# Optimization experiments

Hardware: AMD Instinct MI355X
Metric: run time of the kernel (lower is better)

Reference implementation:

```python
import jax, jax.numpy as jnp
import numpy as np
import math

NUM_HEADS = 8
LN_EPS = 1e-5
SINK_EPS = 1.0  # entropic eps in SinkhornDistance (eps=1)


def _layer_norm(x, g, b):
    m = jnp.mean(x, axis=-1, keepdims=True)
    v = jnp.var(x, axis=-1, keepdims=True)
    return (x - m) * jax.lax.rsqrt(v + LN_EPS) * g + b


def setup_inputs() -> dict:
    key = jax.random.key(0)
    ks = jax.random.split(key, 8)
    B, n, dQ, dV = 8, 1024, 512, 512
    s = 1.0 / math.sqrt(dV)
    return {
        "Q": jax.random.normal(ks[0], (B, n, dQ), jnp.float32),
        "K": jax.random.normal(ks[1], (B, n, dQ), jnp.float32),
        "Wq": jax.random.normal(ks[2], (dV, dQ), jnp.float32) * s,
        "bq": jax.random.normal(ks[3], (dV,), jnp.float32) * 0.01,
        "Wo": jax.random.normal(ks[4], (dV, dV), jnp.float32) * s,
        "bo": jax.random.normal(ks[5], (dV,), jnp.float32) * 0.01,
        "g0": jnp.ones((dV,), jnp.float32),
        "b0": jnp.zeros((dV,), jnp.float32),
        "g1": jnp.ones((dV,), jnp.float32),
        "b1": jnp.zeros((dV,), jnp.float32),
    }


def reference(Q, K, Wq, bq, Wo, bo, g0, b0, g1, b1):
    # K is accepted by the original forward but unused (K_ = V_ = Q_).
    B, n, _ = Q.shape
    dim_V = Wq.shape[0]
    H = NUM_HEADS
    d = dim_V // H

    Qp = Q @ Wq.T + bq                                   # [B, n, dim_V]
    # torch.cat(Q.split(d, 2), 0): head-major stacking -> [H*B, n, d]
    Q_ = Qp.reshape(B, n, H, d).transpose(2, 0, 1, 3).reshape(H * B, n, d)

    sqrtV = math.sqrt(math.sqrt(dim_V))
    X = Q_ / sqrtV
    # cost = dotmat(X, X) = -X X^T  (overall scaled by 1/sqrt(dim_V))
    C = -jnp.einsum('bnd,bmd->bnm', X, X)                # [HB, n, n]

    # log-domain Sinkhorn, eps=1, max_iter=1, mu = nu = 1/n
    log_mu = jnp.log(1.0 / n + 1e-8).astype(Q.dtype)
    M0 = -C / SINK_EPS
    u = SINK_EPS * (log_mu - jax.scipy.special.logsumexp(M0, axis=-1))         # [HB, n]
    v = SINK_EPS * (log_mu - jax.scipy.special.logsumexp(
        (-C + u[:, :, None]) / SINK_EPS, axis=1))                               # [HB, n]
    pi = jnp.exp((-C + u[:, :, None] + v[:, None, :]) / SINK_EPS)               # [HB, n, n]

    A = pi * n
    O_ = Q_ + jnp.einsum('bnm,bmd->bnd', A, Q_)          # [HB, n, d]
    # inverse head stacking -> [B, n, dim_V]
    O = O_.reshape(H, B, n, d).transpose(1, 2, 0, 3).reshape(B, n, dim_V)

    O = _layer_norm(O, g0, b0)
    O = O + jax.nn.relu(O @ Wo.T + bo)
    O = _layer_norm(O, g1, b1)
    return O
```

## Files before the change

### kernel.cpp

```cpp
#include <hip/hip_runtime.h>
#include <hip/hip_bf16.h>

typedef __bf16 bf16;
typedef __bf16 bf16x4 __attribute__((ext_vector_type(4)));
typedef __bf16 bf16x8 __attribute__((ext_vector_type(8)));
typedef float  f32x4  __attribute__((ext_vector_type(4)));

#define DEVI static __device__ __forceinline__

constexpr float SCALE_S = 0.04419417382415922f;
constexpr float LOG_MU  = -6.93146156565f;
constexpr int   LDT     = 72;

DEVI f32x4 mfma16(bf16x8 a, bf16x8 b, f32x4 c) {
    return __builtin_amdgcn_mfma_f32_16x16x32_bf16(a, b, c, 0, 0, 0);
}

DEVI bf16x8 cvt8(const float* __restrict__ p) {
    const float4 f0 = *(const float4*)p;
    const float4 f1 = *(const float4*)(p + 4);
    bf16x8 h;
    h[0] = (bf16)f0.x; h[1] = (bf16)f0.y; h[2] = (bf16)f0.z; h[3] = (bf16)f0.w;
    h[4] = (bf16)f1.x; h[5] = (bf16)f1.y; h[6] = (bf16)f1.z; h[7] = (bf16)f1.w;
    return h;
}

template<int EPI>
__global__ __launch_bounds__(256)
void gemm_kernel(const void* __restrict__ Ap, const float* __restrict__ Bm,
                 const float* __restrict__ bias, const bf16* __restrict__ X0,
                 bf16* __restrict__ outQh, bf16* __restrict__ outQhT,
                 float* __restrict__ outT)
{
    __shared__ bf16 sA[64 * LDT];
    __shared__ bf16 sB[64 * LDT];
    const int tid = threadIdx.x;
    const int rowBase = blockIdx.y * 64;
    const int colBase = blockIdx.x * 64;
    const int w = tid >> 6, lane = tid & 63, quad = lane >> 4, l16 = lane & 15;
    const int wr = (w >> 1) * 32, wc = (w & 1) * 32;

    f32x4 acc[2][2];
    #pragma unroll
    for (int i = 0; i < 2; ++i)
        #pragma unroll
        for (int j = 0; j < 2; ++j)
            #pragma unroll
            for (int e = 0; e < 4; ++e) acc[i][j][e] = 0.f;

    for (int kt = 0; kt < 512; kt += 64) {
        if (kt) __syncthreads();
        #pragma unroll
        for (int it = 0; it < 2; ++it) {
            int idx = it * 256 + tid;
            int r = idx >> 3, kb = idx & 7;
            if (EPI == 0) {
                *(bf16x8*)(&sA[r * LDT + kb * 8]) =
                    cvt8((const float*)Ap + (size_t)(rowBase + r) * 512 + kt + kb * 8);
            } else {
                *(uint4*)(&sA[r * LDT + kb * 8]) =
                    *(const uint4*)((const bf16*)Ap + (size_t)(rowBase + r) * 512 + kt + kb * 8);
            }
            *(bf16x8*)(&sB[r * LDT + kb * 8]) =
                cvt8(Bm + (size_t)(colBase + r) * 512 + kt + kb * 8);
        }
        __syncthreads();
        #pragma unroll
        for (int kk = 0; kk < 2; ++kk) {
            bf16x8 a[2], b[2];
            #pragma unroll
            for (int i = 0; i < 2; ++i)
                a[i] = *(const bf16x8*)(&sA[(wr + i * 16 + l16) * LDT + kk * 32 + quad * 8]);
            #pragma unroll
            for (int j = 0; j < 2; ++j)
                b[j] = *(const bf16x8*)(&sB[(wc + j * 16 + l16) * LDT + kk * 32 + quad * 8]);
            #pragma unroll
            for (int i = 0; i < 2; ++i)
                #pragma unroll
                for (int j = 0; j < 2; ++j)
                    acc[i][j] = mfma16(a[i], b[j], acc[i][j]);
        }
    }

    #pragma unroll
    for (int i = 0; i < 2; ++i) {
        #pragma unroll
        for (int j = 0; j < 2; ++j) {
            const int col = colBase + wc + j * 16 + l16;
            const float bv = bias[col];
            if (EPI == 0) {
                const int hh = col >> 6, jj = col & 63;
                const int rowA = rowBase + wr + i * 16 + quad * 4;
                const int bb = rowA >> 10, iib = rowA & 1023;
                const int bhh = (hh << 3) + bb;
                bf16x4 pk;
                #pragma unroll
                for (int rg = 0; rg < 4; ++rg) {
                    const float z = acc[i][j][rg] + bv;
                    pk[rg] = (bf16)z;
                    outQh[((size_t)(bhh * 1024 + iib + rg) << 6) + jj] = (bf16)z;
                }
                if (outQhT)
                    *(bf16x4*)(&outQhT[(((size_t)bhh * 64 + jj) << 10) + iib]) = pk;
            } else {
                #pragma unroll
                for (int rg = 0; rg < 4; ++rg) {
                    const int row = rowBase + wr + i * 16 + quad * 4 + rg;
                    const float z = acc[i][j][rg] + bv;
                    const float x0 = (float)X0[(size_t)row * 512 + col];
                    outT[(size_t)row * 512 + col] = x0 + fmaxf(z, 0.f);
                }
            }
        }
    }
}

template<int ADD_U>
__global__ __launch_bounds__(256, 4)
void sink_lse_kernel(const bf16* __restrict__ Qh, const float* __restrict__ uin,
                     float* __restrict__ out)
{
    __shared__ bf16 sQi[128 * LDT];
    __shared__ bf16 sQm[2][64 * LDT];
    __shared__ float su[1024];
    const int tid = threadIdx.x;
    const int bh = blockIdx.y;
    const int rowTile = blockIdx.x * 128;
    const bf16* Qb = Qh + ((size_t)bh << 16);

    #pragma unroll
    for (int it = 0; it < 4; ++it) {
        int idx = it * 256 + tid;
        int r = idx >> 3, kb = idx & 7;
        *(uint4*)(&sQi[r * LDT + kb * 8]) =
            *(const uint4*)(Qb + ((rowTile + r) << 6) + kb * 8);
    }
    if (ADD_U)
        *(float4*)(&su[tid * 4]) = *(const float4*)(uin + (bh << 10) + tid * 4);

    const int r0 = tid >> 3, kb0 = tid & 7;
    #pragma unroll
    for (int it = 0; it < 2; ++it)
        *(uint4*)(&sQm[0][(it * 32 + r0) * LDT + kb0 * 8]) =
            *(const uint4*)(Qb + ((it * 32 + r0) << 6) + kb0 * 8);
    __syncthreads();

    const int w = tid >> 6, lane = tid & 63, quad = lane >> 4, l16 = lane & 15;
    float rsum[2][4] = {{0.f,0.f,0.f,0.f},{0.f,0.f,0.f,0.f}};

    for (int mt = 0; mt < 16; ++mt) {
        const int cur = mt & 1;
        uint4 pf[2];
        if (mt < 15) {
            #pragma unroll
            for (int it = 0; it < 2; ++it)
                pf[it] = *(const uint4*)(Qb + (((mt + 1) * 64 + it * 32 + r0) << 6) + kb0 * 8);
        }

        f32x4 acc[2][4];
        #pragma unroll
        for (int a = 0; a < 2; ++a)
            #pragma unroll
            for (int ct = 0; ct < 4; ++ct)
                #pragma unroll
                for (int e = 0; e < 4; ++e) acc[a][ct][e] = 0.f;

        #pragma unroll
        for (int kk = 0; kk < 2; ++kk) {
            bf16x8 afr[2], bfr[4];
            #pragma unroll
            for (int a = 0; a < 2; ++a)
                afr[a] = *(const bf16x8*)(&sQi[(w * 32 + a * 16 + l16) * LDT + kk * 32 + quad * 8]);
            #pragma unroll
            for (int ct = 0; ct < 4; ++ct)
                bfr[ct] = *(const bf16x8*)(&sQm[cur][(ct * 16 + l16) * LDT + kk * 32 + quad * 8]);
            #pragma unroll
            for (int a = 0; a < 2; ++a)
                #pragma unroll
                for (int ct = 0; ct < 4; ++ct)
                    acc[a][ct] = mfma16(afr[a], bfr[ct], acc[a][ct]);
        }
        #pragma unroll
        for (int a = 0; a < 2; ++a)
            #pragma unroll
            for (int ct = 0; ct < 4; ++ct) {
                const float uadd = ADD_U ? su[mt * 64 + ct * 16 + l16] : 0.f;
                #pragma unroll
                for (int rg = 0; rg < 4; ++rg)
                    rsum[a][rg] += __expf(acc[a][ct][rg] * SCALE_S + uadd);
            }

        if (mt < 15) {
            #pragma unroll
            for (int it = 0; it < 2; ++it)
                *(uint4*)(&sQm[cur ^ 1][(it * 32 + r0) * LDT + kb0 * 8]) = pf[it];
        }
        __syncthreads();
    }
    #pragma unroll
    for (int off = 1; off < 16; off <<= 1)
        #pragma unroll
        for (int a = 0; a < 2; ++a)
            #pragma unroll
            for (int rg = 0; rg < 4; ++rg)
                rsum[a][rg] += __shfl_xor(rsum[a][rg], off);

    if (l16 == 0) {
        #pragma unroll
        for (int a = 0; a < 2; ++a)
            #pragma unroll
            for (int rg = 0; rg < 4; ++rg)
                out[(bh << 10) + rowTile + w * 32 + a * 16 + quad * 4 + rg] =
                    LOG_MU - __logf(rsum[a][rg]);
    }
}

template<int USE_T>
__global__ __launch_bounds__(256, 2)
void sink_av_kernel(const bf16* __restrict__ Qh, const bf16* __restrict__ QhT,
                    const float* __restrict__ u, const float* __restrict__ v,
                    float* __restrict__ O)
{
    __shared__ bf16 sQi[128 * LDT];
    __shared__ bf16 sQm[2][64 * LDT];
    __shared__ bf16 sQmT[2][64 * LDT];
    __shared__ bf16 sP[4][32 * LDT];
    __shared__ float sv[1024];
    const int tid = threadIdx.x;
    const int bh = blockIdx.y;
    const int rowTile = blockIdx.x * 128;
    const bf16* Qb = Qh + ((size_t)bh << 16);
    const bf16* QbT = QhT + ((size_t)bh << 16);
    const int w = tid >> 6, lane = tid & 63, quad = lane >> 4, l16 = lane & 15;
    const int r0 = tid >> 3, kb0 = tid & 7;

    #pragma unroll
    for (int it = 0; it < 4; ++it) {
        int idx = it * 256 + tid;
        int r = idx >> 3, kb = idx & 7;
        *(uint4*)(&sQi[r * LDT + kb * 8]) =
            *(const uint4*)(Qb + ((rowTile + r) << 6) + kb * 8);
    }
    *(float4*)(&sv[tid * 4]) = *(const float4*)(v + (bh << 10) + tid * 4);
    float u_r[2][4];
    #pragma unroll
    for (int a = 0; a < 2; ++a)
        #pragma unroll
        for (int rg = 0; rg < 4; ++rg)
            u_r[a][rg] = u[(bh << 10) + rowTile + w * 32 + a * 16 + quad * 4 + rg];

    #pragma unroll
    for (int it = 0; it < 2; ++it) {
        const int r = it * 32 + r0;
        uint4 val = *(const uint4*)(Qb + (r << 6) + kb0 * 8);
        *(uint4*)(&sQm[0][r * LDT + kb0 * 8]) = val;
        if (USE_T) {
            *(uint4*)(&sQmT[0][r * LDT + kb0 * 8]) =
                *(const uint4*)(QbT + (r << 10) + kb0 * 8);
        } else {
            union { uint4 q; bf16 e[8]; } cv; cv.q = val;
            #pragma unroll
            for (int j = 0; j < 8; ++j)
                sQmT[0][(kb0 * 8 + j) * LDT + r] = cv.e[j];
        }
    }
    __syncthreads();

    f32x4 accO[2][4];
    #pragma unroll
    for (int a = 0; a < 2; ++a)
        #pragma unroll
        for (int ct = 0; ct < 4; ++ct)
            #pragma unroll
            for (int e = 0; e < 4; ++e) accO[a][ct][e] = 0.f;

    for (int mt = 0; mt < 16; ++mt) {
        const int cur = mt & 1;
        uint4 pfm[2], pft[2];
        if (mt < 15) {
            #pragma unroll
            for (int it = 0; it < 2; ++it) {
                const int r = it * 32 + r0;
                pfm[it] = *(const uint4*)(Qb + (((mt + 1) * 64 + r) << 6) + kb0 * 8);
                if (USE_T)
                    pft[it] = *(const uint4*)(QbT + (r << 10) + (mt + 1) * 64 + kb0 * 8);
            }
        }

        f32x4 acc[2][4];
        #pragma unroll
        for (int a = 0; a < 2; ++a)
            #pragma unroll
            for (int ct = 0; ct < 4; ++ct)
                #pragma unroll
                for (int e = 0; e < 4; ++e) acc[a][ct][e] = 0.f;

        #pragma unroll
        for (int kk = 0; kk < 2; ++kk) {
            bf16x8 afr[2], bfr[4];
            #pragma unroll
            for (int a = 0; a < 2; ++a)
                afr[a] = *(const bf16x8*)(&sQi[(w * 32 + a * 16 + l16) * LDT + kk * 32 + quad * 8]);
            #pragma unroll
            for (int ct = 0; ct < 4; ++ct)
                bfr[ct] = *(const bf16x8*)(&sQm[cur][(ct * 16 + l16) * LDT + kk * 32 + quad * 8]);
            #pragma unroll
            for (int a = 0; a < 2; ++a)
                #pragma unroll
                for (int ct = 0; ct < 4; ++ct)
                    acc[a][ct] = mfma16(afr[a], bfr[ct], acc[a][ct]);
        }
        #pragma unroll
        for (int a = 0; a < 2; ++a)
            #pragma unroll
            for (int ct = 0; ct < 4; ++ct) {
                const float vv = sv[mt * 64 + ct * 16 + l16];
                #pragma unroll
                for (int rg = 0; rg < 4; ++rg) {
                    const float p = 1024.f * __expf(acc[a][ct][rg] * SCALE_S + u_r[a][rg] + vv);
                    sP[w][(a * 16 + quad * 4 + rg) * LDT + ct * 16 + l16] = (bf16)p;
                }
            }
        #pragma unroll
        for (int kk = 0; kk < 2; ++kk) {
            bf16x8 a2[2], b2[4];
            #pragma unroll
            for (int a = 0; a < 2; ++a)
                a2[a] = *(const bf16x8*)(&sP[w][(a * 16 + l16) * LDT + kk * 32 + quad * 8]);
            #pragma unroll
            for (int ct = 0; ct < 4; ++ct)
                b2[ct] = *(const bf16x8*)(&sQmT[cur][(ct * 16 + l16) * LDT + kk * 32 + quad * 8]);
            #pragma unroll
            for (int a = 0; a < 2; ++a)
                #pragma unroll
                for (int ct = 0; ct < 4; ++ct)
                    accO[a][ct] = mfma16(a2[a], b2[ct], accO[a][ct]);
        }

        if (mt < 15) {
            #pragma unroll
            for (int it = 0; it < 2; ++it) {
                const int r = it * 32 + r0;
                *(uint4*)(&sQm[cur ^ 1][r * LDT + kb0 * 8]) = pfm[it];
                if (USE_T) {
                    *(uint4*)(&sQmT[cur ^ 1][r * LDT + kb0 * 8]) = pft[it];
                } else {
                    union { uint4 q; bf16 e[8]; } cv; cv.q = pfm[it];
                    #pragma unroll
                    for (int j = 0; j < 8; ++j)
                        sQmT[cur ^ 1][(kb0 * 8 + j) * LDT + r] = cv.e[j];
                }
            }
        }
        __syncthreads();
    }

    const int hh = bh >> 3, bb = bh & 7;
    #pragma unroll
    for (int a = 0; a < 2; ++a)
        #pragma unroll
        for (int ct = 0; ct < 4; ++ct) {
            const int dcol = ct * 16 + l16;
            #pragma unroll
            for (int rg = 0; rg < 4; ++rg) {
                const int irow = w * 32 + a * 16 + quad * 4 + rg;
                const float o = (float)sQi[irow * LDT + dcol] + accO[a][ct][rg];
                O[((size_t)(bb * 1024 + rowTile + irow) << 9) + (hh << 6) + dcol] = o;
            }
        }
}

template<typename OutT>
__global__ __launch_bounds__(256)
void ln_kernel(const float* __restrict__ X, const float* __restrict__ g,
               const float* __restrict__ bb, OutT* __restrict__ out)
{
    const int row = blockIdx.x;
    const float* x = X + (size_t)row * 512;
    const float2 v2 = ((const float2*)x)[threadIdx.x];
    float s  = v2.x + v2.y;
    float ss = v2.x * v2.x + v2.y * v2.y;
    #pragma unroll
    for (int off = 32; off; off >>= 1) {
        s  += __shfl_down(s, off);
        ss += __shfl_down(ss, off);
    }
    __shared__ float red[8];
    const int w = threadIdx.x >> 6, lane = threadIdx.x & 63;
    if (lane == 0) { red[w] = s; red[4 + w] = ss; }
    __syncthreads();
    s  = red[0] + red[1] + red[2] + red[3];
    ss = red[4] + red[5] + red[6] + red[7];
    const float mean = s * (1.f / 512.f);
    const float var  = ss * (1.f / 512.f) - mean * mean;
    const float rstd = rsqrtf(var + 1e-5f);
    const int c = threadIdx.x * 2;
    const float y0 = (v2.x - mean) * rstd * g[c]     + bb[c];
    const float y1 = (v2.y - mean) * rstd * g[c + 1] + bb[c + 1];
    out[(size_t)row * 512 + c]     = (OutT)y0;
    out[(size_t)row * 512 + c + 1] = (OutT)y1;
}

extern "C" void kernel_launch(void* const* d_in, const int* in_sizes, int n_in,
                              void* d_out, int out_size, void* d_ws, size_t ws_size,
                              hipStream_t stream)
{
    const float* Q  = (const float*)d_in[0];
    const float* Wq = (const float*)d_in[2];
    const float* bq = (const float*)d_in[3];
    const float* Wo = (const float*)d_in[4];
    const float* bo = (const float*)d_in[5];
    const float* g0 = (const float*)d_in[6];
    const float* b0 = (const float*)d_in[7];
    const float* g1 = (const float*)d_in[8];
    const float* b1 = (const float*)d_in[9];

    char* ws = (char*)d_ws;
    const bool useT = ws_size >= (size_t)34078720;

    bf16 *Qh, *QhT, *X0;
    float *u, *v, *Obuf;
    if (useT) {
        Qh   = (bf16*)ws;
        QhT  = (bf16*)(ws + 8388608);
        X0   = (bf16*)(ws + 8388608);
        u    = (float*)(ws + 16777216);
        v    = (float*)(ws + 17039360);
        Obuf = (float*)(ws + 17301504);
    } else {
        Qh   = (bf16*)ws;
        QhT  = nullptr;
        X0   = (bf16*)ws;
        u    = (float*)(ws + 8388608);
        v    = (float*)(ws + 8650752);
        Obuf = (float*)(ws + 8912896);
    }

    gemm_kernel<0><<<dim3(8, 128), 256, 0, stream>>>(Q, Wq, bq, nullptr, Qh, QhT, nullptr);
    sink_lse_kernel<0><<<dim3(8, 64), 256, 0, stream>>>(Qh, nullptr, u);
    sink_lse_kernel<1><<<dim3(8, 64), 256, 0, stream>>>(Qh, u, v);
    if (useT)
        sink_av_kernel<1><<<dim3(8, 64), 256, 0, stream>>>(Qh, QhT, u, v, Obuf);
    else
        sink_av_kernel<0><<<dim3(8, 64), 256, 0, stream>>>(Qh, Qh, u, v, Obuf);
    ln_kernel<bf16><<<8192, 256, 0, stream>>>(Obuf, g0, b0, X0);
    gemm_kernel<1><<<dim3(8, 128), 256, 0, stream>>>(X0, Wo, bo, X0, nullptr, nullptr, Obuf);
    ln_kernel<float><<<8192, 256, 0, stream>>>(Obuf, g1, b1, (float*)d_out);
}
```

Baseline: 227.5 us.

## Keep Sinkhorn probabilities in registers via 32x32 MFMA and permlane swap

```diff
diff --git a/kernel.cpp b/kernel.cpp
--- a/kernel.cpp
+++ b/kernel.cpp
@@ -5,15 +5,26 @@
 typedef __bf16 bf16x4 __attribute__((ext_vector_type(4)));
 typedef __bf16 bf16x8 __attribute__((ext_vector_type(8)));
 typedef float  f32x4  __attribute__((ext_vector_type(4)));
+typedef float  f32x16 __attribute__((ext_vector_type(16)));
+typedef unsigned int uint32x2 __attribute__((ext_vector_type(2)));
 
 #define DEVI static __device__ __forceinline__
 
 constexpr float SCALE_S = 0.04419417382415922f;
-constexpr float LOG_MU  = -6.93146156565f;
+constexpr float SCALE2  = 0.063758716f;
+constexpr float L2MU    = -9.9999852f;
 constexpr int   LDT     = 72;
 
 DEVI f32x4 mfma16(bf16x8 a, bf16x8 b, f32x4 c) {
     return __builtin_amdgcn_mfma_f32_16x16x32_bf16(a, b, c, 0, 0, 0);
+}
+DEVI f32x16 mfma32(bf16x8 a, bf16x8 b, f32x16 c) {
+    return __builtin_amdgcn_mfma_f32_32x32x16_bf16(a, b, c, 0, 0, 0);
+}
+DEVI unsigned cvtpk(float lo, float hi) {
+    unsigned r;
+    asm("v_cvt_pk_bf16_f32 %0, %1, %2" : "=v"(r) : "v"(lo), "v"(hi));
+    return r;
 }
 
 DEVI bf16x8 cvt8(const float* __restrict__ p) {
@@ -124,8 +135,10 @@
     __shared__ bf16 sQm[2][64 * LDT];
     __shared__ float su[1024];
     const int tid = threadIdx.x;
-    const int bh = blockIdx.y;
-    const int rowTile = blockIdx.x * 128;
+    const int lin = blockIdx.y * 8 + blockIdx.x;
+    const int wk  = ((lin & 7) << 6) | (lin >> 3);
+    const int bh = wk >> 3;
+    const int rowTile = (wk & 7) * 128;
     const bf16* Qb = Qh + ((size_t)bh << 16);
 
     #pragma unroll
@@ -187,7 +200,8 @@
                 const float uadd = ADD_U ? su[mt * 64 + ct * 16 + l16] : 0.f;
                 #pragma unroll
                 for (int rg = 0; rg < 4; ++rg)
-                    rsum[a][rg] += __expf(acc[a][ct][rg] * SCALE_S + uadd);
+                    rsum[a][rg] += __builtin_amdgcn_exp2f(
+                        fmaf(acc[a][ct][rg], SCALE2, uadd));
             }
 
         if (mt < 15) {
@@ -211,7 +225,7 @@
             #pragma unroll
             for (int rg = 0; rg < 4; ++rg)
                 out[(bh << 10) + rowTile + w * 32 + a * 16 + quad * 4 + rg] =
-                    LOG_MU - __logf(rsum[a][rg]);
+                    L2MU - __builtin_amdgcn_logf(rsum[a][rg]);
     }
 }
 
@@ -224,14 +238,15 @@
     __shared__ bf16 sQi[128 * LDT];
     __shared__ bf16 sQm[2][64 * LDT];
     __shared__ bf16 sQmT[2][64 * LDT];
-    __shared__ bf16 sP[4][32 * LDT];
     __shared__ float sv[1024];
     const int tid = threadIdx.x;
-    const int bh = blockIdx.y;
-    const int rowTile = blockIdx.x * 128;
+    const int lin = blockIdx.y * 8 + blockIdx.x;
+    const int wk  = ((lin & 7) << 6) | (lin >> 3);
+    const int bh = wk >> 3;
+    const int rowTile = (wk & 7) * 128;
     const bf16* Qb = Qh + ((size_t)bh << 16);
     const bf16* QbT = QhT + ((size_t)bh << 16);
-    const int w = tid >> 6, lane = tid & 63, quad = lane >> 4, l16 = lane & 15;
+    const int w = tid >> 6, lane = tid & 63, hi = lane >> 5, l31 = lane & 31;
     const int r0 = tid >> 3, kb0 = tid & 7;
 
     #pragma unroll
@@ -242,12 +257,7 @@
             *(const uint4*)(Qb + ((rowTile + r) << 6) + kb * 8);
     }
     *(float4*)(&sv[tid * 4]) = *(const float4*)(v + (bh << 10) + tid * 4);
-    float u_r[2][4];
-    #pragma unroll
-    for (int a = 0; a < 2; ++a)
-        #pragma unroll
-        for (int rg = 0; rg < 4; ++rg)
-            u_r[a][rg] = u[(bh << 10) + rowTile + w * 32 + a * 16 + quad * 4 + rg];
+    const float u2p = u[(bh << 10) + rowTile + w * 32 + l31] + 10.f;
 
     #pragma unroll
     for (int it = 0; it < 2; ++it) {
@@ -266,13 +276,11 @@
     }
     __syncthreads();
 
-    f32x4 accO[2][4];
-    #pragma unroll
-    for (int a = 0; a < 2; ++a)
-        #pragma unroll
-        for (int ct = 0; ct < 4; ++ct)
-            #pragma unroll
-            for (int e = 0; e < 4; ++e) accO[a][ct][e] = 0.f;
+    f32x16 accO[2];
+    #pragma unroll
+    for (int dt = 0; dt < 2; ++dt)
+        #pragma unroll
+        for (int e = 0; e < 16; ++e) accO[dt][e] = 0.f;
 
     for (int mt = 0; mt < 16; ++mt) {
         const int cur = mt & 1;
@@ -287,55 +295,55 @@
             }
         }
 
-        f32x4 acc[2][4];
-        #pragma unroll
-        for (int a = 0; a < 2; ++a)
-            #pragma unroll
-            for (int ct = 0; ct < 4; ++ct)
-                #pragma unroll
-                for (int e = 0; e < 4; ++e) acc[a][ct][e] = 0.f;
-
-        #pragma unroll
-        for (int kk = 0; kk < 2; ++kk) {
-            bf16x8 afr[2], bfr[4];
-            #pragma unroll
-            for (int a = 0; a < 2; ++a)
-                afr[a] = *(const bf16x8*)(&sQi[(w * 32 + a * 16 + l16) * LDT + kk * 32 + quad * 8]);
-            #pragma unroll
-            for (int ct = 0; ct < 4; ++ct)
-                bfr[ct] = *(const bf16x8*)(&sQm[cur][(ct * 16 + l16) * LDT + kk * 32 + quad * 8]);
-            #pragma unroll
-            for (int a = 0; a < 2; ++a)
-                #pragma unroll
-                for (int ct = 0; ct < 4; ++ct)
-                    acc[a][ct] = mfma16(afr[a], bfr[ct], acc[a][ct]);
-        }
-        #pragma unroll
-        for (int a = 0; a < 2; ++a)
-            #pragma unroll
-            for (int ct = 0; ct < 4; ++ct) {
-                const float vv = sv[mt * 64 + ct * 16 + l16];
-                #pragma unroll
-                for (int rg = 0; rg < 4; ++rg) {
-                    const float p = 1024.f * __expf(acc[a][ct][rg] * SCALE_S + u_r[a][rg] + vv);
-                    sP[w][(a * 16 + quad * 4 + rg) * LDT + ct * 16 + l16] = (bf16)p;
-                }
-            }
-        #pragma unroll
-        for (int kk = 0; kk < 2; ++kk) {
-            bf16x8 a2[2], b2[4];
-            #pragma unroll
-            for (int a = 0; a < 2; ++a)
-                a2[a] = *(const bf16x8*)(&sP[w][(a * 16 + l16) * LDT + kk * 32 + quad * 8]);
-            #pragma unroll
-            for (int ct = 0; ct < 4; ++ct)
-                b2[ct] = *(const bf16x8*)(&sQmT[cur][(ct * 16 + l16) * LDT + kk * 32 + quad * 8]);
-            #pragma unroll
-            for (int a = 0; a < 2; ++a)
-                #pragma unroll
-                for (int ct = 0; ct < 4; ++ct)
-                    accO[a][ct] = mfma16(a2[a], b2[ct], accO[a][ct]);
-        }
+        f32x16 accT[2];
+        #pragma unroll
+        for (int t = 0; t < 2; ++t)
+            #pragma unroll
+            for (int e = 0; e < 16; ++e) accT[t][e] = 0.f;
+        #pragma unroll
+        for (int ks = 0; ks < 4; ++ks) {
+            const bf16x8 bq = *(const bf16x8*)(&sQi[(w * 32 + l31) * LDT + ks * 16 + hi * 8]);
+            #pragma unroll
+            for (int t = 0; t < 2; ++t) {
+                const bf16x8 am = *(const bf16x8*)(&sQm[cur][(t * 32 + l31) * LDT + ks * 16 + hi * 8]);
+                accT[t] = mfma32(am, bq, accT[t]);
+            }
+        }
+
+        bf16x8 pa[4];
+        #pragma unroll
+        for (int t = 0; t < 2; ++t) {
+            f32x4 vf[4];
+            #pragma unroll
+            for (int g = 0; g < 4; ++g)
+                vf[g] = *(const f32x4*)(&sv[mt * 64 + t * 32 + g * 8 + hi * 4]);
+            float p[16];
+            #pragma unroll
+            for (int r = 0; r < 16; ++r)
+                p[r] = __builtin_amdgcn_exp2f(
+                         fmaf(accT[t][r], SCALE2, u2p + vf[r >> 2][r & 3]));
+            #pragma unroll
+            for (int kk = 0; kk < 2; ++kk) {
+                const int rb = kk * 8;
+                unsigned X0 = cvtpk(p[rb + 0], p[rb + 1]);
+                unsigned Y0 = cvtpk(p[rb + 4], p[rb + 5]);
+                unsigned X1 = cvtpk(p[rb + 2], p[rb + 3]);
+                unsigned Y1 = cvtpk(p[rb + 6], p[rb + 7]);
+                uint32x2 s0 = __builtin_amdgcn_permlane32_swap(X0, Y0, false, false);
+                uint32x2 s1 = __builtin_amdgcn_permlane32_swap(X1, Y1, false, false);
+                union { unsigned wd[4]; bf16x8 v8; } u4;
+                u4.wd[0] = s0[0]; u4.wd[1] = s1[0]; u4.wd[2] = s0[1]; u4.wd[3] = s1[1];
+                pa[t * 2 + kk] = u4.v8;
+            }
+        }
+
+        #pragma unroll
+        for (int ks = 0; ks < 4; ++ks)
+            #pragma unroll
+            for (int dt = 0; dt < 2; ++dt) {
+                const bf16x8 bt = *(const bf16x8*)(&sQmT[cur][(dt * 32 + l31) * LDT + ks * 16 + hi * 8]);
+                accO[dt] = mfma32(pa[ks], bt, accO[dt]);
+            }
 
         if (mt < 15) {
             #pragma unroll
@@ -357,17 +365,15 @@
 
     const int hh = bh >> 3, bb = bh & 7;
     #pragma unroll
-    for (int a = 0; a < 2; ++a)
-        #pragma unroll
-        for (int ct = 0; ct < 4; ++ct) {
-            const int dcol = ct * 16 + l16;
-            #pragma unroll
-            for (int rg = 0; rg < 4; ++rg) {
-                const int irow = w * 32 + a * 16 + quad * 4 + rg;
-                const float o = (float)sQi[irow * LDT + dcol] + accO[a][ct][rg];
-                O[((size_t)(bb * 1024 + rowTile + irow) << 9) + (hh << 6) + dcol] = o;
-            }
-        }
+    for (int dt = 0; dt < 2; ++dt) {
+        const int dcol = dt * 32 + l31;
+        #pragma unroll
+        for (int r = 0; r < 16; ++r) {
+            const int irow = w * 32 + (r & 3) + 8 * (r >> 2) + 4 * hi;
+            const float o = (float)sQi[irow * LDT + dcol] + accO[dt][r];
+            O[((size_t)(bb * 1024 + rowTile + irow) << 9) + (hh << 6) + dcol] = o;
+        }
+    }
 }
 
 template<typename OutT>
```

Result: faster. 207.8 us (-8.6%).
